# Kernel optimization log

Measured on AMD Instinct MI355X. Metric: run time of the kernel, lower is better.

The kernel has to match this reference:

```python
import jax, jax.numpy as jnp
import numpy as np

NUM_HEADS = 8
ALPHA = 0.01  # leaky_relu slope
MAX_SEQ = 64


def layer_norm(x, g, b, eps=1e-5):
    m = jnp.mean(x, axis=-1, keepdims=True)
    v = jnp.var(x, axis=-1, keepdims=True)
    return (x - m) * jax.lax.rsqrt(v + eps) * g + b


def ff(x, w1, b1, w2, b2):
    # Linear -> exact GELU -> Linear (torch nn.GELU default is erf-based)
    return jax.nn.gelu(x @ w1.T + b1, approximate=False) @ w2.T + b2


def mha(q, k, v, in_w, in_b, out_w, out_b, kpm):
    # torch nn.MultiheadAttention, batch_first=False. q:[Tq,E,d], k/v:[Tk,E,d], kpm:[E,Tk] True=pad
    d = q.shape[-1]
    H = NUM_HEADS
    dh = d // H
    qp = q @ in_w[:d].T + in_b[:d]
    kp = k @ in_w[d:2 * d].T + in_b[d:2 * d]
    vp = v @ in_w[2 * d:].T + in_b[2 * d:]
    Tq, E, _ = qp.shape
    Tk = kp.shape[0]
    qh = qp.reshape(Tq, E, H, dh) * (dh ** -0.5)
    kh = kp.reshape(Tk, E, H, dh)
    vh = vp.reshape(Tk, E, H, dh)
    scores = jnp.einsum('qehd,kehd->ehqk', qh, kh)  # [E,H,Tq,Tk]
    scores = jnp.where(kpm[:, None, None, :], jnp.float32(-1e9), scores)
    att = jax.nn.softmax(scores, axis=-1)
    out = jnp.einsum('ehqk,kehd->qehd', att, vh).reshape(Tq, E, d)
    return out @ out_w.T + out_b


def setup_inputs() -> dict:
    key = jax.random.key(0)
    ks = jax.random.split(key, 40)
    N, d, E, Seq, H = 50000, 64, 150000, 5, NUM_HEADS

    def xn(k, shape, scale):
        return jax.random.normal(k, shape, dtype=jnp.float32) * scale

    inp = {
        'features': xn(ks[0], (N, d), 1.0),
        'pos_emb': xn(ks[1], (MAX_SEQ, d), 0.02),
        'self_in_w': xn(ks[2], (3 * d, d), 0.1),
        'self_in_b': jnp.zeros((3 * d,), jnp.float32),
        'self_out_w': xn(ks[3], (d, d), 0.1),
        'self_out_b': jnp.zeros((d,), jnp.float32),
        'cross_in_w': xn(ks[4], (3 * d, d), 0.1),
        'cross_in_b': jnp.zeros((3 * d,), jnp.float32),
        'cross_out_w': xn(ks[5], (d, d), 0.1),
        'cross_out_b': jnp.zeros((d,), jnp.float32),
        'sa_ln1_g': jnp.ones((d,), jnp.float32), 'sa_ln1_b': jnp.zeros((d,), jnp.float32),
        'sa_ln2_g': jnp.ones((d,), jnp.float32), 'sa_ln2_b': jnp.zeros((d,), jnp.float32),
        'ca_ln1_g': jnp.ones((d,), jnp.float32), 'ca_ln1_b': jnp.zeros((d,), jnp.float32),
        'ca_ln2_g': jnp.ones((d,), jnp.float32), 'ca_ln2_b': jnp.zeros((d,), jnp.float32),
        'sa_ff_w1': xn(ks[6], (4 * d, d), 0.08), 'sa_ff_b1': jnp.zeros((4 * d,), jnp.float32),
        'sa_ff_w2': xn(ks[7], (d, 4 * d), 0.08), 'sa_ff_b2': jnp.zeros((d,), jnp.float32),
        'ca_ff_w1': xn(ks[8], (4 * d, d), 0.08), 'ca_ff_b1': jnp.zeros((4 * d,), jnp.float32),
        'ca_ff_w2': xn(ks[9], (d, 4 * d), 0.08), 'ca_ff_b2': jnp.zeros((d,), jnp.float32),
        'inst_w': xn(ks[10], (NUM_HEADS * d, d), 0.08),
        'attn_vec': xn(ks[11], (1, NUM_HEADS, d), 0.2),
        'edge_metapath_indices': jax.random.randint(ks[12], (E, Seq), 0, N, dtype=jnp.int64)
            if jax.config.jax_enable_x64 else jax.random.randint(ks[12], (E, Seq), 0, N).astype(jnp.int32),
        'dst': jax.random.randint(ks[13], (E,), 0, N).astype(jnp.int32),
    }
    inp['edge_metapath_indices'] = inp['edge_metapath_indices'].astype(jnp.int32)
    return inp


def reference(features, pos_emb, self_in_w, self_in_b, self_out_w, self_out_b,
              cross_in_w, cross_in_b, cross_out_w, cross_out_b,
              sa_ln1_g, sa_ln1_b, sa_ln2_g, sa_ln2_b,
              ca_ln1_g, ca_ln1_b, ca_ln2_g, ca_ln2_b,
              sa_ff_w1, sa_ff_b1, sa_ff_w2, sa_ff_b2,
              ca_ff_w1, ca_ff_b1, ca_ff_w2, ca_ff_b2,
              inst_w, attn_vec, edge_metapath_indices, dst):
    N, d = features.shape
    pad_id = N  # module pads one zero row; indices == pad_id are padding
    feats = jnp.concatenate([features, jnp.zeros((1, d), features.dtype)], axis=0)
    idx = edge_metapath_indices  # [E, Seq]
    E, Seq = idx.shape
    kpm = idx == pad_id  # [E, Seq] key padding mask

    edata = feats[idx]  # [E, Seq, d] gather (embedding)
    tokens = jnp.transpose(edata, (1, 0, 2))  # [Seq, E, d]
    pos_vec = pos_emb[:Seq][:, None, :]  # [Seq, 1, d]
    pos_vec = jnp.where(kpm.T[:, :, None], jnp.float32(0.0), pos_vec)
    tokens = tokens + pos_vec  # pos_drop is identity in eval

    # pre-LN self-attention block over the metapath sequence
    sa_in = layer_norm(tokens, sa_ln1_g, sa_ln1_b)
    tokens = tokens + mha(sa_in, sa_in, sa_in, self_in_w, self_in_b, self_out_w, self_out_b, kpm)
    sa_out = jnp.transpose(tokens, (1, 0, 2))  # [E, Seq, d]

    valid = (~kpm).astype(features.dtype)  # [E, Seq]
    denom = jnp.clip(valid.sum(axis=1, keepdims=True), 1.0, None)
    inst_emb = (sa_out * valid[:, :, None]).sum(axis=1) / denom  # masked mean pool
    inst_emb = inst_emb + ff(layer_norm(inst_emb, sa_ln2_g, sa_ln2_b), sa_ff_w1, sa_ff_b1, sa_ff_w2, sa_ff_b2)

    # cross-attention: last (target) node attends over the sequence
    lengths = (~kpm).sum(axis=1)
    last_pos = jnp.clip(lengths - 1, 0, None)
    last_ids = jnp.take_along_axis(idx, last_pos[:, None], axis=1)[:, 0]
    target_feat = feats[last_ids]
    q = layer_norm(target_feat, ca_ln1_g, ca_ln1_b)[None]  # [1, E, d]
    cross_out = mha(q, tokens, tokens, cross_in_w, cross_in_b, cross_out_w, cross_out_b, kpm)
    inst_emb = inst_emb + cross_out[0]
    inst_emb = inst_emb + ff(layer_norm(inst_emb, ca_ln2_g, ca_ln2_b), ca_ff_w1, ca_ff_b1, ca_ff_w2, ca_ff_b2)

    # heads projection, leaky-relu attention score, edge softmax, scatter-sum
    eft = (inst_emb @ inst_w.T).reshape(E, NUM_HEADS, d)  # [E, H, d]
    a = jnp.sum(eft * attn_vec, axis=-1)  # [E, H]
    a = jnp.where(a > 0, a, ALPHA * a)  # leaky_relu
    seg_max = jax.ops.segment_max(a, dst, num_segments=N)  # per-dst-node max
    a_exp = jnp.exp(a - seg_max[dst])
    seg_sum = jax.ops.segment_sum(a_exp, dst, num_segments=N)
    att = a_exp / seg_sum[dst]  # edge_softmax; attn_drop=0 -> identity
    ret = jax.ops.segment_sum(eft * att[:, :, None], dst, num_segments=N)  # [N, H, d]
    return ret
```

## Files before the change

kernel.cpp:

```cpp
#include <hip/hip_runtime.h>
#include <math.h>

#define D 64
#define LOG2E 1.44269504088896340736f
#define QSCALE (0.35355339059327373f * LOG2E)

typedef float f32x4 __attribute__((ext_vector_type(4)));
typedef float vf4 __attribute__((ext_vector_type(4)));
typedef short bf16x8 __attribute__((ext_vector_type(8)));
typedef unsigned short ushort_t;

#define MF(a, b, c) __builtin_amdgcn_mfma_f32_16x16x32_bf16(a, b, c, 0, 0, 0)

__device__ __forceinline__ float bcast(float x, int i) {
  return __int_as_float(__builtin_amdgcn_readlane(__float_as_int(x), i));
}
__device__ __forceinline__ float qsum(float x) {
  x += __shfl_xor(x, 16);
  x += __shfl_xor(x, 32);
  return x;
}
__device__ __forceinline__ ushort_t f2b(float f) {
  unsigned int u = __float_as_uint(f);
  unsigned int r = (u + 0x7FFFu + ((u >> 16) & 1u)) >> 16;
  return (ushort_t)r;
}
__device__ __forceinline__ float b2f(short s) {
  return __uint_as_float(((unsigned int)(unsigned short)s) << 16);
}
__device__ __forceinline__ f32x4 ld4(const float* __restrict__ p) { return *(const f32x4*)p; }
__device__ __forceinline__ unsigned int fkey(float f) {
  unsigned int b = __float_as_uint(f);
  return (b & 0x80000000u) ? ~b : (b | 0x80000000u);
}
__device__ __forceinline__ float funkey(unsigned int k) {
  return __uint_as_float((k & 0x80000000u) ? (k ^ 0x80000000u) : ~k);
}
__device__ __forceinline__ bf16x8 mkpair(const f32x4& ce, const f32x4& co) {
  bf16x8 b;
#pragma unroll
  for (int j = 0; j < 4; j++) {
    b[j] = (short)f2b(ce[j]);
    b[4 + j] = (short)f2b(co[j]);
  }
  return b;
}
__device__ __forceinline__ f32x4 unpk(bf16x8 p, int half) {
  f32x4 r;
#pragma unroll
  for (int j = 0; j < 4; j++) r[j] = b2f(p[half * 4 + j]);
  return r;
}

__device__ __forceinline__ void lnT(const f32x4 (&x)[4], f32x4 (&y)[4],
                                    const float* __restrict__ g, const float* __restrict__ b,
                                    int quad) {
  float s1 = 0.f, s2 = 0.f;
#pragma unroll
  for (int ct = 0; ct < 4; ct++)
#pragma unroll
    for (int r = 0; r < 4; r++) { s1 += x[ct][r]; s2 += x[ct][r] * x[ct][r]; }
  s1 = qsum(s1);
  s2 = qsum(s2);
  float mean = s1 * 0.015625f;
  float var = s2 * 0.015625f - mean * mean;
  float rs = rsqrtf(var + 1e-5f);
#pragma unroll
  for (int ct = 0; ct < 4; ct++) {
    f32x4 gv = ld4(g + 16 * ct + 4 * quad);
    f32x4 bv = ld4(b + 16 * ct + 4 * quad);
#pragma unroll
    for (int r = 0; r < 4; r++) y[ct][r] = (x[ct][r] - mean) * rs * gv[r] + bv[r];
  }
}

__global__ void zero_kernel(float4* __restrict__ p, int n4) {
  int t = blockIdx.x * blockDim.x + threadIdx.x;
  if (t < n4) p[t] = make_float4(0.f, 0.f, 0.f, 0.f);
}

__global__ void prep_kernel(const float* __restrict__ si, const float* __restrict__ so,
                            const float* __restrict__ w1s, const float* __restrict__ w2s,
                            const float* __restrict__ ci, const float* __restrict__ co,
                            const float* __restrict__ w1c, const float* __restrict__ w2c,
                            const float* __restrict__ iw, const float* __restrict__ av,
                            float* __restrict__ ws) {
  int t = blockIdx.x * blockDim.x + threadIdx.x;
  ushort_t* bw = (ushort_t*)(ws + 33280);
  if (t < 98304) {
    const float* src;
    int base, cs;
    int l = t;
    if      (l < 12288) { src = si;  base = 0;     cs = 6; }
    else if (l < 16384) { src = so;  base = 12288; cs = 6; l -= 12288; }
    else if (l < 32768) { src = w1s; base = 16384; cs = 6; l -= 16384; }
    else if (l < 49152) { src = w2s; base = 32768; cs = 8; l -= 32768; }
    else if (l < 61440) { src = ci;  base = 49152; cs = 6; l -= 49152; }
    else if (l < 65536) { src = co;  base = 61440; cs = 6; l -= 61440; }
    else if (l < 81920) { src = w1c; base = 65536; cs = 6; l -= 65536; }
    else                { src = w2c; base = 81920; cs = 8; l -= 81920; }
    int c = l >> cs, k = l & ((1 << cs) - 1);
    int T = (1 << cs) >> 5;
    int ct = c >> 4, m = c & 15, tt = k >> 5, rem = k & 31;
    int quad = (rem >> 2) & 3;
    int j = (((rem >> 4) & 1) << 2) | (rem & 3);
    bw[base + (size_t)((ct * T + tt) * 64 + quad * 16 + m) * 8 + j] = f2b(src[l]);
  } else if (t < 131072) {
    int l = t - 98304;
    int c = l >> 6, k = l & 63;
    ws[(k >> 2) * 2048 + c * 4 + (k & 3)] = iw[l];
  } else if (t < 131584) {
    int l = t - 131072;
    int h = l >> 6, k = l & 63;
    float acc = 0.f;
    for (int c = 0; c < 64; c++) acc += av[h * 64 + c] * iw[(h * 64 + c) * 64 + k];
    ws[32768 + h * 64 + k] = acc;
  }
}

__device__ __forceinline__ void ffnT(f32x4 (&inst)[4],
                                     const float* __restrict__ g, const float* __restrict__ b,
                                     const bf16x8* __restrict__ W1, const bf16x8* __restrict__ W2,
                                     const float* __restrict__ b1, const float* __restrict__ b2,
                                     int lane, int quad) {
  f32x4 y[4];
  lnT(inst, y, g, b, quad);
  bf16x8 x0 = mkpair(y[0], y[1]), x1 = mkpair(y[2], y[3]);
  bf16x8 Hp[8];
#pragma unroll
  for (int ht = 0; ht < 8; ht++) {
    f32x4 h[2];
#pragma unroll
    for (int u = 0; u < 2; u++) {
      int ct = 2 * ht + u;
      f32x4 c = {0.f, 0.f, 0.f, 0.f};
      c = MF(W1[(ct * 2 + 0) * 64 + lane], x0, c);
      c = MF(W1[(ct * 2 + 1) * 64 + lane], x1, c);
      f32x4 bb = ld4(b1 + 16 * ct + 4 * quad);
#pragma unroll
      for (int r = 0; r < 4; r++) {
        float v = c[r] + bb[r];
        h[u][r] = 0.5f * v * (1.0f + erff(v * 0.70710678118654752440f));
      }
    }
    Hp[ht] = mkpair(h[0], h[1]);
  }
#pragma unroll
  for (int ct = 0; ct < 4; ct++) {
    f32x4 c = {0.f, 0.f, 0.f, 0.f};
#pragma unroll
    for (int t = 0; t < 8; t++) c = MF(W2[(ct * 8 + t) * 64 + lane], Hp[t], c);
    f32x4 bb = ld4(b2 + 16 * ct + 4 * quad);
#pragma unroll
    for (int r = 0; r < 4; r++) inst[ct][r] += c[r] + bb[r];
  }
}

__global__ __launch_bounds__(64, 2)
void edge_kernel(const float* __restrict__ features, const float* __restrict__ pos_emb,
                 const float* __restrict__ self_in_b, const float* __restrict__ self_out_b,
                 const float* __restrict__ cross_in_b, const float* __restrict__ cross_out_b,
                 const float* __restrict__ sa_ln1_g, const float* __restrict__ sa_ln1_b,
                 const float* __restrict__ sa_ln2_g, const float* __restrict__ sa_ln2_b,
                 const float* __restrict__ ca_ln1_g, const float* __restrict__ ca_ln1_b,
                 const float* __restrict__ ca_ln2_g, const float* __restrict__ ca_ln2_b,
                 const float* __restrict__ sa_ff_b1, const float* __restrict__ sa_ff_b2,
                 const float* __restrict__ ca_ff_b1, const float* __restrict__ ca_ff_b2,
                 const int* __restrict__ midx, const int* __restrict__ dstv,
                 const float* __restrict__ ws,
                 float* __restrict__ inst_out, float* __restrict__ a_out,
                 unsigned int* __restrict__ seg_max, int E, int N) {
  const int lane = threadIdx.x;
  const int quad = lane >> 4, lo = lane & 15;
  const int e0 = blockIdx.x * 16;
  __shared__ float xp[16 * 68];

  const ushort_t* bw = (const ushort_t*)(ws + 33280);
  const bf16x8* WSI = (const bf16x8*)(bw);
  const bf16x8* WSO = (const bf16x8*)(bw + 12288);
  const bf16x8* W1S = (const bf16x8*)(bw + 16384);
  const bf16x8* W2S = (const bf16x8*)(bw + 32768);
  const bf16x8* WCI = (const bf16x8*)(bw + 49152);
  const bf16x8* WCO = (const bf16x8*)(bw + 61440);
  const bf16x8* W1C = (const bf16x8*)(bw + 65536);
  const bf16x8* W2C = (const bf16x8*)(bw + 81920);
  const float* uvec = ws + 32768;

  const bool ge = (e0 + lo) < E;
  const int eIdx = min(e0 + lo, E - 1);
  int ids[5];
#pragma unroll
  for (int s = 0; s < 5; s++) ids[s] = midx[eIdx * 5 + s];
  int vb = 0;
#pragma unroll
  for (int s = 0; s < 5; s++)
    if (ids[s] != N && ge) vb |= (1 << s);
  const int nv = __popc(vb);
  const int lp = max(nv - 1, 0);
  int lid = ids[0];
#pragma unroll
  for (int s = 1; s < 5; s++) lid = (lp == s) ? ids[s] : lid;

  bf16x8 XL[5][2];
#pragma unroll
  for (int s = 0; s < 5; s++) {
    f32x4 t[4], y[4];
    const bool vd = (vb >> s) & 1;
    const float* fp = features + (size_t)min(ids[s], N - 1) * 64;
#pragma unroll
    for (int ct = 0; ct < 4; ct++) {
      f32x4 f = ld4(fp + 16 * ct + 4 * quad);
      f32x4 p = ld4(pos_emb + s * 64 + 16 * ct + 4 * quad);
#pragma unroll
      for (int r = 0; r < 4; r++) t[ct][r] = vd ? (f[r] + p[r]) : 0.f;
    }
    lnT(t, y, sa_ln1_g, sa_ln1_b, quad);
    XL[s][0] = mkpair(y[0], y[1]);
    XL[s][1] = mkpair(y[2], y[3]);
  }

  bf16x8 Kp[5][2], Vp[5][2];
#pragma unroll
  for (int s = 0; s < 5; s++) {
    f32x4 kt[4], vt[4];
#pragma unroll
    for (int ct = 0; ct < 4; ct++) {
      f32x4 c = {0.f, 0.f, 0.f, 0.f};
      c = MF(WSI[((4 + ct) * 2 + 0) * 64 + lane], XL[s][0], c);
      c = MF(WSI[((4 + ct) * 2 + 1) * 64 + lane], XL[s][1], c);
      f32x4 bb = ld4(self_in_b + 64 + 16 * ct + 4 * quad);
#pragma unroll
      for (int r = 0; r < 4; r++) kt[ct][r] = c[r] + bb[r];
      f32x4 c2 = {0.f, 0.f, 0.f, 0.f};
      c2 = MF(WSI[((8 + ct) * 2 + 0) * 64 + lane], XL[s][0], c2);
      c2 = MF(WSI[((8 + ct) * 2 + 1) * 64 + lane], XL[s][1], c2);
      f32x4 bb2 = ld4(self_in_b + 128 + 16 * ct + 4 * quad);
#pragma unroll
      for (int r = 0; r < 4; r++) vt[ct][r] = c2[r] + bb2[r];
    }
    Kp[s][0] = mkpair(kt[0], kt[1]);
    Kp[s][1] = mkpair(kt[2], kt[3]);
    Vp[s][0] = mkpair(vt[0], vt[1]);
    Vp[s][1] = mkpair(vt[2], vt[3]);
  }

  f32x4 pool[4];
#pragma unroll
  for (int ct = 0; ct < 4; ct++) pool[ct] = (f32x4){0.f, 0.f, 0.f, 0.f};
  bf16x8 TP[5][2];
#pragma unroll
  for (int qs = 0; qs < 5; qs++) {
    f32x4 qf[4];
#pragma unroll
    for (int ct = 0; ct < 4; ct++) {
      f32x4 c = {0.f, 0.f, 0.f, 0.f};
      c = MF(WSI[(ct * 2 + 0) * 64 + lane], XL[qs][0], c);
      c = MF(WSI[(ct * 2 + 1) * 64 + lane], XL[qs][1], c);
      f32x4 bb = ld4(self_in_b + 16 * ct + 4 * quad);
#pragma unroll
      for (int r = 0; r < 4; r++) qf[ct][r] = (c[r] + bb[r]) * QSCALE;
    }
    float p[4][5];
#pragma unroll
    for (int ct = 0; ct < 4; ct++) {
      float mx = -3.0e30f;
#pragma unroll
      for (int ks = 0; ks < 5; ks++) {
        f32x4 kv = unpk(Kp[ks][ct >> 1], ct & 1);
        float sp = qf[ct][0] * kv[0] + qf[ct][1] * kv[1] + qf[ct][2] * kv[2] + qf[ct][3] * kv[3];
        sp += __shfl_xor(sp, 16);
        float sv = ((vb >> ks) & 1) ? sp : -1e30f;
        p[ct][ks] = sv;
        mx = fmaxf(mx, sv);
      }
      float sum = 0.f;
#pragma unroll
      for (int ks = 0; ks < 5; ks++) { p[ct][ks] = exp2f(p[ct][ks] - mx); sum += p[ct][ks]; }
      float ri = 1.0f / sum;
#pragma unroll
      for (int ks = 0; ks < 5; ks++) p[ct][ks] *= ri;
    }
    f32x4 o[4];
#pragma unroll
    for (int ct = 0; ct < 4; ct++) {
      o[ct] = (f32x4){0.f, 0.f, 0.f, 0.f};
#pragma unroll
      for (int ks = 0; ks < 5; ks++) {
        f32x4 vv = unpk(Vp[ks][ct >> 1], ct & 1);
#pragma unroll
        for (int r = 0; r < 4; r++) o[ct][r] = fmaf(p[ct][ks], vv[r], o[ct][r]);
      }
    }
    bf16x8 o0 = mkpair(o[0], o[1]), o1 = mkpair(o[2], o[3]);
    const bool vd = (vb >> qs) & 1;
    const float* fp = features + (size_t)min(ids[qs], N - 1) * 64;
    f32x4 tpc[4];
#pragma unroll
    for (int ct = 0; ct < 4; ct++) {
      f32x4 c = {0.f, 0.f, 0.f, 0.f};
      c = MF(WSO[(ct * 2 + 0) * 64 + lane], o0, c);
      c = MF(WSO[(ct * 2 + 1) * 64 + lane], o1, c);
      f32x4 bb = ld4(self_out_b + 16 * ct + 4 * quad);
      f32x4 f = ld4(fp + 16 * ct + 4 * quad);
      f32x4 pp = ld4(pos_emb + qs * 64 + 16 * ct + 4 * quad);
#pragma unroll
      for (int r = 0; r < 4; r++) {
        float tokr = vd ? (f[r] + pp[r]) : 0.f;
        float tp = c[r] + bb[r] + tokr;
        tpc[ct][r] = tp;
        pool[ct][r] += vd ? tp : 0.f;
      }
    }
    TP[qs][0] = mkpair(tpc[0], tpc[1]);
    TP[qs][1] = mkpair(tpc[2], tpc[3]);
  }

  f32x4 inst[4];
  {
    float rn = 1.0f / (float)max(nv, 1);
#pragma unroll
    for (int ct = 0; ct < 4; ct++)
#pragma unroll
      for (int r = 0; r < 4; r++) inst[ct][r] = pool[ct][r] * rn;
  }

  ffnT(inst, sa_ln2_g, sa_ln2_b, W1S, W2S, sa_ff_b1, sa_ff_b2, lane, quad);

  {
    f32x4 tf[4], xq[4];
    const bool vdl = lid != N;
    const float* fp = features + (size_t)min(lid, N - 1) * 64;
#pragma unroll
    for (int ct = 0; ct < 4; ct++) {
      f32x4 f = ld4(fp + 16 * ct + 4 * quad);
#pragma unroll
      for (int r = 0; r < 4; r++) tf[ct][r] = vdl ? f[r] : 0.f;
    }
    lnT(tf, xq, ca_ln1_g, ca_ln1_b, quad);
    bf16x8 xq0 = mkpair(xq[0], xq[1]), xq1 = mkpair(xq[2], xq[3]);
    f32x4 qcf[4];
#pragma unroll
    for (int ct = 0; ct < 4; ct++) {
      f32x4 c = {0.f, 0.f, 0.f, 0.f};
      c = MF(WCI[(ct * 2 + 0) * 64 + lane], xq0, c);
      c = MF(WCI[(ct * 2 + 1) * 64 + lane], xq1, c);
      f32x4 bb = ld4(cross_in_b + 16 * ct + 4 * quad);
#pragma unroll
      for (int r = 0; r < 4; r++) qcf[ct][r] = (c[r] + bb[r]) * QSCALE;
    }
    bf16x8 Kc[5][2], Vc[5][2];
#pragma unroll
    for (int s = 0; s < 5; s++) {
      f32x4 kt[4], vt[4];
#pragma unroll
      for (int ct = 0; ct < 4; ct++) {
        f32x4 c = {0.f, 0.f, 0.f, 0.f};
        c = MF(WCI[((4 + ct) * 2 + 0) * 64 + lane], TP[s][0], c);
        c = MF(WCI[((4 + ct) * 2 + 1) * 64 + lane], TP[s][1], c);
        f32x4 bb = ld4(cross_in_b + 64 + 16 * ct + 4 * quad);
#pragma unroll
        for (int r = 0; r < 4; r++) kt[ct][r] = c[r] + bb[r];
        f32x4 c2 = {0.f, 0.f, 0.f, 0.f};
        c2 = MF(WCI[((8 + ct) * 2 + 0) * 64 + lane], TP[s][0], c2);
        c2 = MF(WCI[((8 + ct) * 2 + 1) * 64 + lane], TP[s][1], c2);
        f32x4 bb2 = ld4(cross_in_b + 128 + 16 * ct + 4 * quad);
#pragma unroll
        for (int r = 0; r < 4; r++) vt[ct][r] = c2[r] + bb2[r];
      }
      Kc[s][0] = mkpair(kt[0], kt[1]);
      Kc[s][1] = mkpair(kt[2], kt[3]);
      Vc[s][0] = mkpair(vt[0], vt[1]);
      Vc[s][1] = mkpair(vt[2], vt[3]);
    }
    float p[4][5];
#pragma unroll
    for (int ct = 0; ct < 4; ct++) {
      float mx = -3.0e30f;
#pragma unroll
      for (int ks = 0; ks < 5; ks++) {
        f32x4 kv = unpk(Kc[ks][ct >> 1], ct & 1);
        float sp = qcf[ct][0] * kv[0] + qcf[ct][1] * kv[1] + qcf[ct][2] * kv[2] + qcf[ct][3] * kv[3];
        sp += __shfl_xor(sp, 16);
        float sv = ((vb >> ks) & 1) ? sp : -1e30f;
        p[ct][ks] = sv;
        mx = fmaxf(mx, sv);
      }
      float sum = 0.f;
#pragma unroll
      for (int ks = 0; ks < 5; ks++) { p[ct][ks] = exp2f(p[ct][ks] - mx); sum += p[ct][ks]; }
      float ri = 1.0f / sum;
#pragma unroll
      for (int ks = 0; ks < 5; ks++) p[ct][ks] *= ri;
    }
    f32x4 co[4];
#pragma unroll
    for (int ct = 0; ct < 4; ct++) {
      co[ct] = (f32x4){0.f, 0.f, 0.f, 0.f};
#pragma unroll
      for (int ks = 0; ks < 5; ks++) {
        f32x4 vv = unpk(Vc[ks][ct >> 1], ct & 1);
#pragma unroll
        for (int r = 0; r < 4; r++) co[ct][r] = fmaf(p[ct][ks], vv[r], co[ct][r]);
      }
    }
    bf16x8 c0 = mkpair(co[0], co[1]), c1 = mkpair(co[2], co[3]);
#pragma unroll
    for (int ct = 0; ct < 4; ct++) {
      f32x4 c = {0.f, 0.f, 0.f, 0.f};
      c = MF(WCO[(ct * 2 + 0) * 64 + lane], c0, c);
      c = MF(WCO[(ct * 2 + 1) * 64 + lane], c1, c);
      f32x4 bb = ld4(cross_out_b + 16 * ct + 4 * quad);
#pragma unroll
      for (int r = 0; r < 4; r++) inst[ct][r] += c[r] + bb[r];
    }
  }

  ffnT(inst, ca_ln2_g, ca_ln2_b, W1C, W2C, ca_ff_b1, ca_ff_b2, lane, quad);

  float a8[8];
#pragma unroll
  for (int h = 0; h < 8; h++) {
    float sp = 0.f;
#pragma unroll
    for (int ct = 0; ct < 4; ct++) {
      f32x4 uu = ld4(uvec + h * 64 + 16 * ct + 4 * quad);
#pragma unroll
      for (int r = 0; r < 4; r++) sp = fmaf(inst[ct][r], uu[r], sp);
    }
    sp = qsum(sp);
    a8[h] = sp > 0.f ? sp : 0.01f * sp;
  }
  if (ge) {
    int dd = dstv[e0 + lo];
    float v0 = quad == 0 ? a8[0] : quad == 1 ? a8[2] : quad == 2 ? a8[4] : a8[6];
    float v1 = quad == 0 ? a8[1] : quad == 1 ? a8[3] : quad == 2 ? a8[5] : a8[7];
    atomicMax(&seg_max[dd * 8 + 2 * quad], fkey(v0));
    atomicMax(&seg_max[dd * 8 + 2 * quad + 1], fkey(v1));
    if (quad < 2) {
      f32x4 st = (quad == 0) ? (f32x4){a8[0], a8[1], a8[2], a8[3]}
                             : (f32x4){a8[4], a8[5], a8[6], a8[7]};
      *(f32x4*)(a_out + (size_t)(e0 + lo) * 8 + 4 * quad) = st;
    }
  }

#pragma unroll
  for (int ct = 0; ct < 4; ct++)
    *(f32x4*)(&xp[lo * 68 + 16 * ct + 4 * quad]) = inst[ct];
  __syncthreads();
  {
    int er = lane >> 2, cb = (lane & 3) * 16;
    if (e0 + er < E) {
#pragma unroll
      for (int u = 0; u < 4; u++) {
        f32x4 v = *(const f32x4*)(&xp[er * 68 + cb + 4 * u]);
        *(f32x4*)(inst_out + (size_t)(e0 + er) * 64 + cb + 4 * u) = v;
      }
    }
  }
}

__global__ void expsum_kernel(const float* __restrict__ a, const int* __restrict__ dstv,
                              const unsigned int* __restrict__ seg_max,
                              float* __restrict__ seg_sum, int E8) {
  int t = blockIdx.x * blockDim.x + threadIdx.x;
  if (t >= E8) return;
  int e = t >> 3, h = t & 7;
  int dd = dstv[e];
  float m = funkey(seg_max[dd * 8 + h]);
  atomicAdd(&seg_sum[dd * 8 + h], __expf(a[t] - m));
}

__global__ __launch_bounds__(256)
void scatter_kernel(const float* __restrict__ inst_emb, const float* __restrict__ a,
                    const unsigned int* __restrict__ seg_max, const float* __restrict__ seg_sum,
                    const int* __restrict__ dstv, float* __restrict__ out, int E) {
  const int wid = (blockIdx.x * blockDim.x + threadIdx.x) >> 6;
  const int lane = threadIdx.x & 63;
  if (wid >= E) return;
  int dd = dstv[wid];
  float iv = inst_emb[(size_t)wid * D + lane];
#pragma unroll
  for (int h = 0; h < 8; h++) {
    float m = funkey(seg_max[dd * 8 + h]);
    float s = seg_sum[dd * 8 + h];
    float att = __expf(a[wid * 8 + h] - m) / s;
    atomicAdd(&out[(size_t)dd * 512 + h * 64 + lane], att * iv);
  }
}

__global__ __launch_bounds__(256)
void head_transform_kernel(const float* __restrict__ T_iw, float* __restrict__ out, int N) {
  const int wid = (blockIdx.x * blockDim.x + threadIdx.x) >> 6;
  const int lane = threadIdx.x & 63;
  const int h = wid & 7;
  const int n0 = (wid >> 3) * 4;
  if (n0 >= N) return;
  float z[4], acc[4];
#pragma unroll
  for (int j = 0; j < 4; j++) {
    z[j] = (n0 + j < N) ? out[((size_t)(n0 + j) * 8 + h) * D + lane] : 0.f;
    acc[j] = 0.f;
  }
  const vf4* P = (const vf4*)T_iw;
  for (int k4 = 0; k4 < 16; k4++) {
    vf4 w = P[k4 * 512 + h * 64 + lane];
#pragma unroll
    for (int u = 0; u < 4; u++) {
      int i = k4 * 4 + u;
#pragma unroll
      for (int j = 0; j < 4; j++) acc[j] = fmaf(bcast(z[j], i), w[u], acc[j]);
    }
  }
#pragma unroll
  for (int j = 0; j < 4; j++)
    if (n0 + j < N) out[((size_t)(n0 + j) * 8 + h) * D + lane] = acc[j];
}

extern "C" void kernel_launch(void* const* d_in, const int* in_sizes, int n_in,
                              void* d_out, int out_size, void* d_ws, size_t ws_size,
                              hipStream_t stream) {
  const float* features   = (const float*)d_in[0];
  const float* pos_emb    = (const float*)d_in[1];
  const float* self_in_w  = (const float*)d_in[2];
  const float* self_in_b  = (const float*)d_in[3];
  const float* self_out_w = (const float*)d_in[4];
  const float* self_out_b = (const float*)d_in[5];
  const float* cross_in_w = (const float*)d_in[6];
  const float* cross_in_b = (const float*)d_in[7];
  const float* cross_out_w= (const float*)d_in[8];
  const float* cross_out_b= (const float*)d_in[9];
  const float* sa_ln1_g = (const float*)d_in[10];
  const float* sa_ln1_b = (const float*)d_in[11];
  const float* sa_ln2_g = (const float*)d_in[12];
  const float* sa_ln2_b = (const float*)d_in[13];
  const float* ca_ln1_g = (const float*)d_in[14];
  const float* ca_ln1_b = (const float*)d_in[15];
  const float* ca_ln2_g = (const float*)d_in[16];
  const float* ca_ln2_b = (const float*)d_in[17];
  const float* sa_ff_w1 = (const float*)d_in[18];
  const float* sa_ff_b1 = (const float*)d_in[19];
  const float* sa_ff_w2 = (const float*)d_in[20];
  const float* sa_ff_b2 = (const float*)d_in[21];
  const float* ca_ff_w1 = (const float*)d_in[22];
  const float* ca_ff_b1 = (const float*)d_in[23];
  const float* ca_ff_w2 = (const float*)d_in[24];
  const float* ca_ff_b2 = (const float*)d_in[25];
  const float* inst_w   = (const float*)d_in[26];
  const float* attn_vec = (const float*)d_in[27];
  const int* midx = (const int*)d_in[28];
  const int* dstv = (const int*)d_in[29];

  const int N = in_sizes[0] / 64;
  const int E = in_sizes[29];

  float* wsf = (float*)d_ws;
  float* inst_emb = wsf + 131072;
  float* a_arr = inst_emb + (size_t)E * 64;
  unsigned int* seg_max = (unsigned int*)(a_arr + (size_t)E * 8);
  float* seg_sum = (float*)(seg_max + (size_t)N * 8);

  {
    int n4 = out_size / 4;
    zero_kernel<<<(n4 + 255) / 256, 256, 0, stream>>>((float4*)d_out, n4);
    int s4 = (N * 16) / 4;
    zero_kernel<<<(s4 + 255) / 256, 256, 0, stream>>>((float4*)seg_max, s4);
  }

  prep_kernel<<<(131584 + 255) / 256, 256, 0, stream>>>(
      self_in_w, self_out_w, sa_ff_w1, sa_ff_w2, cross_in_w, cross_out_w, ca_ff_w1, ca_ff_w2,
      inst_w, attn_vec, wsf);

  int nblk = (E + 15) / 16;
  edge_kernel<<<nblk, 64, 0, stream>>>(
      features, pos_emb, self_in_b, self_out_b, cross_in_b, cross_out_b, sa_ln1_g, sa_ln1_b,
      sa_ln2_g, sa_ln2_b, ca_ln1_g, ca_ln1_b, ca_ln2_g, ca_ln2_b, sa_ff_b1, sa_ff_b2, ca_ff_b1,
      ca_ff_b2, midx, dstv, wsf, inst_emb, a_arr, seg_max, E, N);

  expsum_kernel<<<(E * 8 + 255) / 256, 256, 0, stream>>>(a_arr, dstv, seg_max, seg_sum, E * 8);

  scatter_kernel<<<(E + 3) / 4, 256, 0, stream>>>(inst_emb, a_arr, seg_max, seg_sum, dstv,
                                                  (float*)d_out, E);

  int hwave = ((N + 3) / 4) * 8;
  head_transform_kernel<<<(hwave + 3) / 4, 256, 0, stream>>>(wsf, (float*)d_out, N);
}
```

Measured before the change: 1.024 ms.

## Recompute layer-norm inputs per stage and macro-unroll to cut register pressure

New measurement: 1.071 ms. +4.6%, slower.

```diff
diff --git a/kernel.cpp b/kernel.cpp
--- a/kernel.cpp
+++ b/kernel.cpp
@@ -118,6 +118,158 @@
   }
 }
 
+#define SC1(KARR, QF, CT, KS, P)                                                        \
+  { f32x4 kv_ = unpk(KARR[KS][(CT) >> 1], (CT) & 1);                                    \
+    float sp_ = QF[CT][0] * kv_[0] + QF[CT][1] * kv_[1] + QF[CT][2] * kv_[2] +          \
+                QF[CT][3] * kv_[3];                                                     \
+    sp_ += __shfl_xor(sp_, 16);                                                         \
+    P = ((vb >> (KS)) & 1) ? sp_ : -1e30f; }
+
+#define PV1(VARR, CT, KS, P, ACC)                                                       \
+  { f32x4 vv_ = unpk(VARR[KS][(CT) >> 1], (CT) & 1);                                    \
+    _Pragma("unroll") for (int r = 0; r < 4; r++) ACC[r] = fmaf(P, vv_[r], ACC[r]); }
+
+#define ATT_CT(KARR, VARR, QF, CT, OD)                                                  \
+  {                                                                                     \
+    float p0, p1, p2, p3, p4;                                                           \
+    SC1(KARR, QF, CT, 0, p0); SC1(KARR, QF, CT, 1, p1); SC1(KARR, QF, CT, 2, p2);       \
+    SC1(KARR, QF, CT, 3, p3); SC1(KARR, QF, CT, 4, p4);                                 \
+    float mx_ = fmaxf(fmaxf(fmaxf(p0, p1), fmaxf(p2, p3)), p4);                         \
+    p0 = exp2f(p0 - mx_); p1 = exp2f(p1 - mx_); p2 = exp2f(p2 - mx_);                   \
+    p3 = exp2f(p3 - mx_); p4 = exp2f(p4 - mx_);                                         \
+    float ri_ = 1.0f / (p0 + p1 + p2 + p3 + p4);                                        \
+    p0 *= ri_; p1 *= ri_; p2 *= ri_; p3 *= ri_; p4 *= ri_;                              \
+    OD = (f32x4){0.f, 0.f, 0.f, 0.f};                                                   \
+    PV1(VARR, CT, 0, p0, OD); PV1(VARR, CT, 1, p1, OD); PV1(VARR, CT, 2, p2, OD);       \
+    PV1(VARR, CT, 3, p3, OD); PV1(VARR, CT, 4, p4, OD);                                 \
+  }
+
+#define KV_STAGE(S)                                                                     \
+  {                                                                                     \
+    f32x4 t[4], y[4];                                                                   \
+    const bool vd = (vb >> (S)) & 1;                                                    \
+    const float* fp = features + (size_t)min(ids[S], N - 1) * 64;                       \
+    _Pragma("unroll")                                                                   \
+    for (int ct = 0; ct < 4; ct++) {                                                    \
+      f32x4 f = ld4(fp + 16 * ct + 4 * quad);                                           \
+      f32x4 pv = ld4(pos_emb + (S) * 64 + 16 * ct + 4 * quad);                          \
+      _Pragma("unroll")                                                                 \
+      for (int r = 0; r < 4; r++) t[ct][r] = vd ? (f[r] + pv[r]) : 0.f;                 \
+    }                                                                                   \
+    lnT(t, y, sa_ln1_g, sa_ln1_b, quad);                                                \
+    bf16x8 xl0 = mkpair(y[0], y[1]), xl1 = mkpair(y[2], y[3]);                          \
+    f32x4 kt[4], vt[4];                                                                 \
+    _Pragma("unroll")                                                                   \
+    for (int ct = 0; ct < 4; ct++) {                                                    \
+      f32x4 c = {0.f, 0.f, 0.f, 0.f};                                                   \
+      c = MF(WSI[((4 + ct) * 2 + 0) * 64 + lane], xl0, c);                              \
+      c = MF(WSI[((4 + ct) * 2 + 1) * 64 + lane], xl1, c);                              \
+      f32x4 bb = ld4(self_in_b + 64 + 16 * ct + 4 * quad);                              \
+      _Pragma("unroll")                                                                 \
+      for (int r = 0; r < 4; r++) kt[ct][r] = c[r] + bb[r];                             \
+      f32x4 c2 = {0.f, 0.f, 0.f, 0.f};                                                  \
+      c2 = MF(WSI[((8 + ct) * 2 + 0) * 64 + lane], xl0, c2);                            \
+      c2 = MF(WSI[((8 + ct) * 2 + 1) * 64 + lane], xl1, c2);                            \
+      f32x4 bb2 = ld4(self_in_b + 128 + 16 * ct + 4 * quad);                            \
+      _Pragma("unroll")                                                                 \
+      for (int r = 0; r < 4; r++) vt[ct][r] = c2[r] + bb2[r];                           \
+    }                                                                                   \
+    Kp[S][0] = mkpair(kt[0], kt[1]); Kp[S][1] = mkpair(kt[2], kt[3]);                   \
+    Vp[S][0] = mkpair(vt[0], vt[1]); Vp[S][1] = mkpair(vt[2], vt[3]);                   \
+  }
+
+#define Q_STAGE(S)                                                                      \
+  {                                                                                     \
+    const bool vd = (vb >> (S)) & 1;                                                    \
+    const float* fp = features + (size_t)min(ids[S], N - 1) * 64;                       \
+    f32x4 t[4], y[4];                                                                   \
+    _Pragma("unroll")                                                                   \
+    for (int ct = 0; ct < 4; ct++) {                                                    \
+      f32x4 f = ld4(fp + 16 * ct + 4 * quad);                                           \
+      f32x4 pv = ld4(pos_emb + (S) * 64 + 16 * ct + 4 * quad);                          \
+      _Pragma("unroll")                                                                 \
+      for (int r = 0; r < 4; r++) t[ct][r] = vd ? (f[r] + pv[r]) : 0.f;                 \
+    }                                                                                   \
+    lnT(t, y, sa_ln1_g, sa_ln1_b, quad);                                                \
+    bf16x8 xl0 = mkpair(y[0], y[1]), xl1 = mkpair(y[2], y[3]);                          \
+    f32x4 qf[4];                                                                        \
+    _Pragma("unroll")                                                                   \
+    for (int ct = 0; ct < 4; ct++) {                                                    \
+      f32x4 c = {0.f, 0.f, 0.f, 0.f};                                                   \
+      c = MF(WSI[(ct * 2 + 0) * 64 + lane], xl0, c);                                    \
+      c = MF(WSI[(ct * 2 + 1) * 64 + lane], xl1, c);                                    \
+      f32x4 bb = ld4(self_in_b + 16 * ct + 4 * quad);                                   \
+      _Pragma("unroll")                                                                 \
+      for (int r = 0; r < 4; r++) qf[ct][r] = (c[r] + bb[r]) * QSCALE;                  \
+    }                                                                                   \
+    f32x4 oa0, oa1, oa2, oa3;                                                           \
+    ATT_CT(Kp, Vp, qf, 0, oa0); ATT_CT(Kp, Vp, qf, 1, oa1);                             \
+    ATT_CT(Kp, Vp, qf, 2, oa2); ATT_CT(Kp, Vp, qf, 3, oa3);                             \
+    bf16x8 op0 = mkpair(oa0, oa1), op1 = mkpair(oa2, oa3);                              \
+    f32x4 tpc[4];                                                                       \
+    _Pragma("unroll")                                                                   \
+    for (int ct = 0; ct < 4; ct++) {                                                    \
+      f32x4 c = {0.f, 0.f, 0.f, 0.f};                                                   \
+      c = MF(WSO[(ct * 2 + 0) * 64 + lane], op0, c);                                    \
+      c = MF(WSO[(ct * 2 + 1) * 64 + lane], op1, c);                                    \
+      f32x4 bb = ld4(self_out_b + 16 * ct + 4 * quad);                                  \
+      _Pragma("unroll")                                                                 \
+      for (int r = 0; r < 4; r++) {                                                     \
+        float tp_ = c[r] + bb[r] + t[ct][r];                                            \
+        tpc[ct][r] = tp_;                                                               \
+        pool[ct][r] += vd ? tp_ : 0.f;                                                  \
+      }                                                                                 \
+    }                                                                                   \
+    TP[S][0] = mkpair(tpc[0], tpc[1]); TP[S][1] = mkpair(tpc[2], tpc[3]);               \
+  }
+
+#define CKV_STAGE(S)                                                                    \
+  {                                                                                     \
+    f32x4 kt[4], vt[4];                                                                 \
+    _Pragma("unroll")                                                                   \
+    for (int ct = 0; ct < 4; ct++) {                                                    \
+      f32x4 c = {0.f, 0.f, 0.f, 0.f};                                                   \
+      c = MF(WCI[((4 + ct) * 2 + 0) * 64 + lane], TP[S][0], c);                         \
+      c = MF(WCI[((4 + ct) * 2 + 1) * 64 + lane], TP[S][1], c);                         \
+      f32x4 bb = ld4(cross_in_b + 64 + 16 * ct + 4 * quad);                             \
+      _Pragma("unroll")                                                                 \
+      for (int r = 0; r < 4; r++) kt[ct][r] = c[r] + bb[r];                             \
+      f32x4 c2 = {0.f, 0.f, 0.f, 0.f};                                                  \
+      c2 = MF(WCI[((8 + ct) * 2 + 0) * 64 + lane], TP[S][0], c2);                       \
+      c2 = MF(WCI[((8 + ct) * 2 + 1) * 64 + lane], TP[S][1], c2);                       \
+      f32x4 bb2 = ld4(cross_in_b + 128 + 16 * ct + 4 * quad);                           \
+      _Pragma("unroll")                                                                 \
+      for (int r = 0; r < 4; r++) vt[ct][r] = c2[r] + bb2[r];                           \
+    }                                                                                   \
+    Kc[S][0] = mkpair(kt[0], kt[1]); Kc[S][1] = mkpair(kt[2], kt[3]);                   \
+    Vc[S][0] = mkpair(vt[0], vt[1]); Vc[S][1] = mkpair(vt[2], vt[3]);                   \
+  }
+
+#define FF_H2(CT, HD)                                                                   \
+  { f32x4 c = {0.f, 0.f, 0.f, 0.f};                                                     \
+    c = MF(W1[((CT) * 2 + 0) * 64 + lane], x0, c);                                      \
+    c = MF(W1[((CT) * 2 + 1) * 64 + lane], x1, c);                                      \
+    f32x4 bb = ld4(b1 + 16 * (CT) + 4 * quad);                                          \
+    _Pragma("unroll")                                                                   \
+    for (int r = 0; r < 4; r++) {                                                       \
+      float v = c[r] + bb[r];                                                           \
+      HD[r] = 0.5f * v * (1.0f + erff(v * 0.70710678118654752440f));                    \
+    } }
+
+#define FF_O(CT)                                                                        \
+  { f32x4 c = {0.f, 0.f, 0.f, 0.f};                                                     \
+    c = MF(W2[((CT) * 8 + 0) * 64 + lane], Hp0, c);                                     \
+    c = MF(W2[((CT) * 8 + 1) * 64 + lane], Hp1, c);                                     \
+    c = MF(W2[((CT) * 8 + 2) * 64 + lane], Hp2, c);                                     \
+    c = MF(W2[((CT) * 8 + 3) * 64 + lane], Hp3, c);                                     \
+    c = MF(W2[((CT) * 8 + 4) * 64 + lane], Hp4, c);                                     \
+    c = MF(W2[((CT) * 8 + 5) * 64 + lane], Hp5, c);                                     \
+    c = MF(W2[((CT) * 8 + 6) * 64 + lane], Hp6, c);                                     \
+    c = MF(W2[((CT) * 8 + 7) * 64 + lane], Hp7, c);                                     \
+    f32x4 bb = ld4(b2 + 16 * (CT) + 4 * quad);                                          \
+    _Pragma("unroll")                                                                   \
+    for (int r = 0; r < 4; r++) inst[CT][r] += c[r] + bb[r]; }
+
 __device__ __forceinline__ void ffnT(f32x4 (&inst)[4],
                                      const float* __restrict__ g, const float* __restrict__ b,
                                      const bf16x8* __restrict__ W1, const bf16x8* __restrict__ W2,
@@ -126,35 +278,28 @@
   f32x4 y[4];
   lnT(inst, y, g, b, quad);
   bf16x8 x0 = mkpair(y[0], y[1]), x1 = mkpair(y[2], y[3]);
-  bf16x8 Hp[8];
-#pragma unroll
-  for (int ht = 0; ht < 8; ht++) {
-    f32x4 h[2];
-#pragma unroll
-    for (int u = 0; u < 2; u++) {
-      int ct = 2 * ht + u;
-      f32x4 c = {0.f, 0.f, 0.f, 0.f};
-      c = MF(W1[(ct * 2 + 0) * 64 + lane], x0, c);
-      c = MF(W1[(ct * 2 + 1) * 64 + lane], x1, c);
-      f32x4 bb = ld4(b1 + 16 * ct + 4 * quad);
-#pragma unroll
-      for (int r = 0; r < 4; r++) {
-        float v = c[r] + bb[r];
-        h[u][r] = 0.5f * v * (1.0f + erff(v * 0.70710678118654752440f));
-      }
-    }
-    Hp[ht] = mkpair(h[0], h[1]);
-  }
-#pragma unroll
-  for (int ct = 0; ct < 4; ct++) {
-    f32x4 c = {0.f, 0.f, 0.f, 0.f};
-#pragma unroll
-    for (int t = 0; t < 8; t++) c = MF(W2[(ct * 8 + t) * 64 + lane], Hp[t], c);
-    f32x4 bb = ld4(b2 + 16 * ct + 4 * quad);
-#pragma unroll
-    for (int r = 0; r < 4; r++) inst[ct][r] += c[r] + bb[r];
-  }
-}
+  f32x4 ha, hb;
+  FF_H2(0, ha);  FF_H2(1, hb);  bf16x8 Hp0 = mkpair(ha, hb);
+  FF_H2(2, ha);  FF_H2(3, hb);  bf16x8 Hp1 = mkpair(ha, hb);
+  FF_H2(4, ha);  FF_H2(5, hb);  bf16x8 Hp2 = mkpair(ha, hb);
+  FF_H2(6, ha);  FF_H2(7, hb);  bf16x8 Hp3 = mkpair(ha, hb);
+  FF_H2(8, ha);  FF_H2(9, hb);  bf16x8 Hp4 = mkpair(ha, hb);
+  FF_H2(10, ha); FF_H2(11, hb); bf16x8 Hp5 = mkpair(ha, hb);
+  FF_H2(12, ha); FF_H2(13, hb); bf16x8 Hp6 = mkpair(ha, hb);
+  FF_H2(14, ha); FF_H2(15, hb); bf16x8 Hp7 = mkpair(ha, hb);
+  FF_O(0); FF_O(1); FF_O(2); FF_O(3);
+}
+
+#define ASC(H)                                                                          \
+  { float sp = 0.f;                                                                     \
+    _Pragma("unroll")                                                                   \
+    for (int ct = 0; ct < 4; ct++) {                                                    \
+      f32x4 uu = ld4(uvec + (H) * 64 + 16 * ct + 4 * quad);                             \
+      _Pragma("unroll")                                                                 \
+      for (int r = 0; r < 4; r++) sp = fmaf(inst[ct][r], uu[r], sp);                    \
+    }                                                                                   \
+    sp = qsum(sp);                                                                      \
+    a##H = sp > 0.f ? sp : 0.01f * sp; }
 
 __global__ __launch_bounds__(64, 2)
 void edge_kernel(const float* __restrict__ features, const float* __restrict__ pos_emb,
@@ -189,131 +334,33 @@
   const bool ge = (e0 + lo) < E;
   const int eIdx = min(e0 + lo, E - 1);
   int ids[5];
-#pragma unroll
-  for (int s = 0; s < 5; s++) ids[s] = midx[eIdx * 5 + s];
+  ids[0] = midx[eIdx * 5 + 0];
+  ids[1] = midx[eIdx * 5 + 1];
+  ids[2] = midx[eIdx * 5 + 2];
+  ids[3] = midx[eIdx * 5 + 3];
+  ids[4] = midx[eIdx * 5 + 4];
   int vb = 0;
-#pragma unroll
-  for (int s = 0; s < 5; s++)
-    if (ids[s] != N && ge) vb |= (1 << s);
+  if (ids[0] != N && ge) vb |= 1;
+  if (ids[1] != N && ge) vb |= 2;
+  if (ids[2] != N && ge) vb |= 4;
+  if (ids[3] != N && ge) vb |= 8;
+  if (ids[4] != N && ge) vb |= 16;
   const int nv = __popc(vb);
   const int lp = max(nv - 1, 0);
   int lid = ids[0];
-#pragma unroll
-  for (int s = 1; s < 5; s++) lid = (lp == s) ? ids[s] : lid;
-
-  bf16x8 XL[5][2];
-#pragma unroll
-  for (int s = 0; s < 5; s++) {
-    f32x4 t[4], y[4];
-    const bool vd = (vb >> s) & 1;
-    const float* fp = features + (size_t)min(ids[s], N - 1) * 64;
-#pragma unroll
-    for (int ct = 0; ct < 4; ct++) {
-      f32x4 f = ld4(fp + 16 * ct + 4 * quad);
-      f32x4 p = ld4(pos_emb + s * 64 + 16 * ct + 4 * quad);
-#pragma unroll
-      for (int r = 0; r < 4; r++) t[ct][r] = vd ? (f[r] + p[r]) : 0.f;
-    }
-    lnT(t, y, sa_ln1_g, sa_ln1_b, quad);
-    XL[s][0] = mkpair(y[0], y[1]);
-    XL[s][1] = mkpair(y[2], y[3]);
-  }
+  lid = (lp == 1) ? ids[1] : lid;
+  lid = (lp == 2) ? ids[2] : lid;
+  lid = (lp == 3) ? ids[3] : lid;
+  lid = (lp == 4) ? ids[4] : lid;
 
   bf16x8 Kp[5][2], Vp[5][2];
-#pragma unroll
-  for (int s = 0; s < 5; s++) {
-    f32x4 kt[4], vt[4];
-#pragma unroll
-    for (int ct = 0; ct < 4; ct++) {
-      f32x4 c = {0.f, 0.f, 0.f, 0.f};
-      c = MF(WSI[((4 + ct) * 2 + 0) * 64 + lane], XL[s][0], c);
-      c = MF(WSI[((4 + ct) * 2 + 1) * 64 + lane], XL[s][1], c);
-      f32x4 bb = ld4(self_in_b + 64 + 16 * ct + 4 * quad);
-#pragma unroll
-      for (int r = 0; r < 4; r++) kt[ct][r] = c[r] + bb[r];
-      f32x4 c2 = {0.f, 0.f, 0.f, 0.f};
-      c2 = MF(WSI[((8 + ct) * 2 + 0) * 64 + lane], XL[s][0], c2);
-      c2 = MF(WSI[((8 + ct) * 2 + 1) * 64 + lane], XL[s][1], c2);
-      f32x4 bb2 = ld4(self_in_b + 128 + 16 * ct + 4 * quad);
-#pragma unroll
-      for (int r = 0; r < 4; r++) vt[ct][r] = c2[r] + bb2[r];
-    }
-    Kp[s][0] = mkpair(kt[0], kt[1]);
-    Kp[s][1] = mkpair(kt[2], kt[3]);
-    Vp[s][0] = mkpair(vt[0], vt[1]);
-    Vp[s][1] = mkpair(vt[2], vt[3]);
-  }
+  KV_STAGE(0); KV_STAGE(1); KV_STAGE(2); KV_STAGE(3); KV_STAGE(4);
 
   f32x4 pool[4];
 #pragma unroll
   for (int ct = 0; ct < 4; ct++) pool[ct] = (f32x4){0.f, 0.f, 0.f, 0.f};
   bf16x8 TP[5][2];
-#pragma unroll
-  for (int qs = 0; qs < 5; qs++) {
-    f32x4 qf[4];
-#pragma unroll
-    for (int ct = 0; ct < 4; ct++) {
-      f32x4 c = {0.f, 0.f, 0.f, 0.f};
-      c = MF(WSI[(ct * 2 + 0) * 64 + lane], XL[qs][0], c);
-      c = MF(WSI[(ct * 2 + 1) * 64 + lane], XL[qs][1], c);
-      f32x4 bb = ld4(self_in_b + 16 * ct + 4 * quad);
-#pragma unroll
-      for (int r = 0; r < 4; r++) qf[ct][r] = (c[r] + bb[r]) * QSCALE;
-    }
-    float p[4][5];
-#pragma unroll
-    for (int ct = 0; ct < 4; ct++) {
-      float mx = -3.0e30f;
-#pragma unroll
-      for (int ks = 0; ks < 5; ks++) {
-        f32x4 kv = unpk(Kp[ks][ct >> 1], ct & 1);
-        float sp = qf[ct][0] * kv[0] + qf[ct][1] * kv[1] + qf[ct][2] * kv[2] + qf[ct][3] * kv[3];
-        sp += __shfl_xor(sp, 16);
-        float sv = ((vb >> ks) & 1) ? sp : -1e30f;
-        p[ct][ks] = sv;
-        mx = fmaxf(mx, sv);
-      }
-      float sum = 0.f;
-#pragma unroll
-      for (int ks = 0; ks < 5; ks++) { p[ct][ks] = exp2f(p[ct][ks] - mx); sum += p[ct][ks]; }
-      float ri = 1.0f / sum;
-#pragma unroll
-      for (int ks = 0; ks < 5; ks++) p[ct][ks] *= ri;
-    }
-    f32x4 o[4];
-#pragma unroll
-    for (int ct = 0; ct < 4; ct++) {
-      o[ct] = (f32x4){0.f, 0.f, 0.f, 0.f};
-#pragma unroll
-      for (int ks = 0; ks < 5; ks++) {
-        f32x4 vv = unpk(Vp[ks][ct >> 1], ct & 1);
-#pragma unroll
-        for (int r = 0; r < 4; r++) o[ct][r] = fmaf(p[ct][ks], vv[r], o[ct][r]);
-      }
-    }
-    bf16x8 o0 = mkpair(o[0], o[1]), o1 = mkpair(o[2], o[3]);
-    const bool vd = (vb >> qs) & 1;
-    const float* fp = features + (size_t)min(ids[qs], N - 1) * 64;
-    f32x4 tpc[4];
-#pragma unroll
-    for (int ct = 0; ct < 4; ct++) {
-      f32x4 c = {0.f, 0.f, 0.f, 0.f};
-      c = MF(WSO[(ct * 2 + 0) * 64 + lane], o0, c);
-      c = MF(WSO[(ct * 2 + 1) * 64 + lane], o1, c);
-      f32x4 bb = ld4(self_out_b + 16 * ct + 4 * quad);
-      f32x4 f = ld4(fp + 16 * ct + 4 * quad);
-      f32x4 pp = ld4(pos_emb + qs * 64 + 16 * ct + 4 * quad);
-#pragma unroll
-      for (int r = 0; r < 4; r++) {
-        float tokr = vd ? (f[r] + pp[r]) : 0.f;
-        float tp = c[r] + bb[r] + tokr;
-        tpc[ct][r] = tp;
-        pool[ct][r] += vd ? tp : 0.f;
-      }
-    }
-    TP[qs][0] = mkpair(tpc[0], tpc[1]);
-    TP[qs][1] = mkpair(tpc[2], tpc[3]);
-  }
+  Q_STAGE(0); Q_STAGE(1); Q_STAGE(2); Q_STAGE(3); Q_STAGE(4);
 
   f32x4 inst[4];
   {
@@ -349,66 +396,16 @@
       for (int r = 0; r < 4; r++) qcf[ct][r] = (c[r] + bb[r]) * QSCALE;
     }
     bf16x8 Kc[5][2], Vc[5][2];
-#pragma unroll
-    for (int s = 0; s < 5; s++) {
-      f32x4 kt[4], vt[4];
-#pragma unroll
-      for (int ct = 0; ct < 4; ct++) {
-        f32x4 c = {0.f, 0.f, 0.f, 0.f};
-        c = MF(WCI[((4 + ct) * 2 + 0) * 64 + lane], TP[s][0], c);
-        c = MF(WCI[((4 + ct) * 2 + 1) * 64 + lane], TP[s][1], c);
-        f32x4 bb = ld4(cross_in_b + 64 + 16 * ct + 4 * quad);
-#pragma unroll
-        for (int r = 0; r < 4; r++) kt[ct][r] = c[r] + bb[r];
-        f32x4 c2 = {0.f, 0.f, 0.f, 0.f};
-        c2 = MF(WCI[((8 + ct) * 2 + 0) * 64 + lane], TP[s][0], c2);
-        c2 = MF(WCI[((8 + ct) * 2 + 1) * 64 + lane], TP[s][1], c2);
-        f32x4 bb2 = ld4(cross_in_b + 128 + 16 * ct + 4 * quad);
-#pragma unroll
-        for (int r = 0; r < 4; r++) vt[ct][r] = c2[r] + bb2[r];
-      }
-      Kc[s][0] = mkpair(kt[0], kt[1]);
-      Kc[s][1] = mkpair(kt[2], kt[3]);
-      Vc[s][0] = mkpair(vt[0], vt[1]);
-      Vc[s][1] = mkpair(vt[2], vt[3]);
-    }
-    float p[4][5];
-#pragma unroll
-    for (int ct = 0; ct < 4; ct++) {
-      float mx = -3.0e30f;
-#pragma unroll
-      for (int ks = 0; ks < 5; ks++) {
-        f32x4 kv = unpk(Kc[ks][ct >> 1], ct & 1);
-        float sp = qcf[ct][0] * kv[0] + qcf[ct][1] * kv[1] + qcf[ct][2] * kv[2] + qcf[ct][3] * kv[3];
-        sp += __shfl_xor(sp, 16);
-        float sv = ((vb >> ks) & 1) ? sp : -1e30f;
-        p[ct][ks] = sv;
-        mx = fmaxf(mx, sv);
-      }
-      float sum = 0.f;
-#pragma unroll
-      for (int ks = 0; ks < 5; ks++) { p[ct][ks] = exp2f(p[ct][ks] - mx); sum += p[ct][ks]; }
-      float ri = 1.0f / sum;
-#pragma unroll
-      for (int ks = 0; ks < 5; ks++) p[ct][ks] *= ri;
-    }
-    f32x4 co[4];
-#pragma unroll
-    for (int ct = 0; ct < 4; ct++) {
-      co[ct] = (f32x4){0.f, 0.f, 0.f, 0.f};
-#pragma unroll
-      for (int ks = 0; ks < 5; ks++) {
-        f32x4 vv = unpk(Vc[ks][ct >> 1], ct & 1);
-#pragma unroll
-        for (int r = 0; r < 4; r++) co[ct][r] = fmaf(p[ct][ks], vv[r], co[ct][r]);
-      }
-    }
-    bf16x8 c0 = mkpair(co[0], co[1]), c1 = mkpair(co[2], co[3]);
+    CKV_STAGE(0); CKV_STAGE(1); CKV_STAGE(2); CKV_STAGE(3); CKV_STAGE(4);
+    f32x4 cc0, cc1, cc2, cc3;
+    ATT_CT(Kc, Vc, qcf, 0, cc0); ATT_CT(Kc, Vc, qcf, 1, cc1);
+    ATT_CT(Kc, Vc, qcf, 2, cc2); ATT_CT(Kc, Vc, qcf, 3, cc3);
+    bf16x8 cp0 = mkpair(cc0, cc1), cp1 = mkpair(cc2, cc3);
 #pragma unroll
     for (int ct = 0; ct < 4; ct++) {
       f32x4 c = {0.f, 0.f, 0.f, 0.f};
-      c = MF(WCO[(ct * 2 + 0) * 64 + lane], c0, c);
-      c = MF(WCO[(ct * 2 + 1) * 64 + lane], c1, c);
+      c = MF(WCO[(ct * 2 + 0) * 64 + lane], cp0, c);
+      c = MF(WCO[(ct * 2 + 1) * 64 + lane], cp1, c);
       f32x4 bb = ld4(cross_out_b + 16 * ct + 4 * quad);
 #pragma unroll
       for (int r = 0; r < 4; r++) inst[ct][r] += c[r] + bb[r];
@@ -417,28 +414,16 @@
 
   ffnT(inst, ca_ln2_g, ca_ln2_b, W1C, W2C, ca_ff_b1, ca_ff_b2, lane, quad);
 
-  float a8[8];
-#pragma unroll
-  for (int h = 0; h < 8; h++) {
-    float sp = 0.f;
-#pragma unroll
-    for (int ct = 0; ct < 4; ct++) {
-      f32x4 uu = ld4(uvec + h * 64 + 16 * ct + 4 * quad);
-#pragma unroll
-      for (int r = 0; r < 4; r++) sp = fmaf(inst[ct][r], uu[r], sp);
-    }
-    sp = qsum(sp);
-    a8[h] = sp > 0.f ? sp : 0.01f * sp;
-  }
+  float a0, a1, a2, a3, a4, a5, a6, a7;
+  ASC(0); ASC(1); ASC(2); ASC(3); ASC(4); ASC(5); ASC(6); ASC(7);
   if (ge) {
     int dd = dstv[e0 + lo];
-    float v0 = quad == 0 ? a8[0] : quad == 1 ? a8[2] : quad == 2 ? a8[4] : a8[6];
-    float v1 = quad == 0 ? a8[1] : quad == 1 ? a8[3] : quad == 2 ? a8[5] : a8[7];
+    float v0 = quad == 0 ? a0 : quad == 1 ? a2 : quad == 2 ? a4 : a6;
+    float v1 = quad == 0 ? a1 : quad == 1 ? a3 : quad == 2 ? a5 : a7;
     atomicMax(&seg_max[dd * 8 + 2 * quad], fkey(v0));
     atomicMax(&seg_max[dd * 8 + 2 * quad + 1], fkey(v1));
     if (quad < 2) {
-      f32x4 st = (quad == 0) ? (f32x4){a8[0], a8[1], a8[2], a8[3]}
-                             : (f32x4){a8[4], a8[5], a8[6], a8[7]};
+      f32x4 st = (quad == 0) ? (f32x4){a0, a1, a2, a3} : (f32x4){a4, a5, a6, a7};
       *(f32x4*)(a_out + (size_t)(e0 + lo) * 8 + 4 * quad) = st;
     }
   }
```
